# Kernel optimization log

Hardware: AMD Instinct MI355X
Metric: run time of the kernel (lower is better)

## Reference

```python
import jax, jax.numpy as jnp
import numpy as np

B, S, E, H = 4, 2048, 768, 12
D = E // H  # head_dim = 64


def setup_inputs() -> dict:
    key = jax.random.key(0)
    k1, k2, k3 = jax.random.split(key, 3)
    x = jax.random.normal(k1, (B, S, E), dtype=jnp.float32)
    # torch Linear(E, 3E): weight [3E, E]; we store transposed [E, 3E] for x @ W
    W_qkv = jax.random.normal(k2, (E, 3 * E), dtype=jnp.float32) * (E ** -0.5)
    b_qkv = jax.random.normal(k3, (3 * E,), dtype=jnp.float32) * 0.02
    return {"x": x, "W_qkv": W_qkv, "b_qkv": b_qkv}


def reference(x, W_qkv, b_qkv):
    n, length, embed_dim = x.shape
    qkv = x @ W_qkv + b_qkv                                   # [B, S, 3E]
    qkv = qkv.reshape(n, length, 3, H, D).transpose(2, 0, 3, 1, 4)  # [3, B, H, S, D]
    q, k, v = qkv[0], qkv[1], qkv[2]
    scores = jnp.einsum('bhsd,bhtd->bhst', q, k) * (D ** -0.5)  # [B, H, S, S]
    attn = jax.nn.softmax(scores, axis=-1)
    out = jnp.einsum('bhst,bhtd->bhsd', attn, v)               # [B, H, S, D]
    return out.transpose(0, 2, 1, 3).reshape(n, length, embed_dim)
```

## Files before the change

### kernel.cpp

```cpp
#include <hip/hip_runtime.h>
#include <cmath>

#define B_ 4
#define S_ 2048
#define E_ 768
#define H_ 12
#define D_ 64
#define NE3 (3*E_)
#define QKV_ELEMS ((size_t)B_*H_*S_*D_)

typedef __attribute__((ext_vector_type(8)))  short bf16x8;
typedef __attribute__((ext_vector_type(4)))  float f32x4;
typedef __attribute__((ext_vector_type(16))) float f32x16;

__device__ __forceinline__ unsigned short f2bf(float f) {
    union { float f; unsigned u; } v; v.f = f;
    return (unsigned short)((v.u + 0x7FFFu + ((v.u >> 16) & 1u)) >> 16);
}
__device__ __forceinline__ unsigned pk2(float a, float b) {
    return (unsigned)f2bf(a) | ((unsigned)f2bf(b) << 16);
}

__global__ __launch_bounds__(256)
void cvt_x(const float* __restrict__ x, unsigned short* __restrict__ xb)
{
    const size_t i = ((size_t)blockIdx.x * 256 + threadIdx.x) * 8;
    float4 a = *(const float4*)(x + i);
    float4 b = *(const float4*)(x + i + 4);
    ushort4 o0, o1;
    o0.x = f2bf(a.x); o0.y = f2bf(a.y); o0.z = f2bf(a.z); o0.w = f2bf(a.w);
    o1.x = f2bf(b.x); o1.y = f2bf(b.y); o1.z = f2bf(b.z); o1.w = f2bf(b.w);
    *(ushort4*)(xb + i)     = o0;
    *(ushort4*)(xb + i + 4) = o1;
}

__global__ __launch_bounds__(256)
void transpose_w(const float* __restrict__ W, unsigned short* __restrict__ Wt)
{
    __shared__ float t[32][33];
    const int tx = threadIdx.x & 31;
    const int ty = threadIdx.x >> 5;
    const int n0 = blockIdx.x * 32;
    const int k0 = blockIdx.y * 32;
    #pragma unroll
    for (int r = 0; r < 4; ++r)
        t[ty + 8*r][tx] = W[(size_t)(k0 + ty + 8*r) * NE3 + n0 + tx];
    __syncthreads();
    #pragma unroll
    for (int r = 0; r < 4; ++r)
        Wt[(size_t)(n0 + ty + 8*r) * E_ + k0 + tx] = f2bf(t[tx][ty + 8*r]);
}

__global__ __launch_bounds__(256, 2)
void qkv_gemm_mfma(const unsigned short* __restrict__ xb,
                   const unsigned short* __restrict__ Wt,
                   const float* __restrict__ bias,
                   unsigned short* __restrict__ qkv)
{
    __shared__ __align__(16) unsigned short As[128*64];
    __shared__ __align__(16) unsigned short Bs[128*64];

    const int tid  = threadIdx.x;
    const int lane = tid & 63;
    const int wave = tid >> 6;
    const int lo   = lane & 15;
    const int hi   = lane >> 4;
    const int wr   = wave >> 1;
    const int wc   = wave & 1;
    const int nstart = blockIdx.x * 128;
    const int mstart = blockIdx.y * 128;

    f32x4 acc[4][4];
    #pragma unroll
    for (int i = 0; i < 4; ++i)
        #pragma unroll
        for (int j = 0; j < 4; ++j) acc[i][j] = (f32x4){0.f,0.f,0.f,0.f};

    for (int k0 = 0; k0 < E_; k0 += 64) {
        __syncthreads();
        #pragma unroll
        for (int it = 0; it < 4; ++it) {
            const int cid = tid + it*256;
            const int row = cid >> 3, c = cid & 7;
            bf16x8 av = *(const bf16x8*)(xb + (size_t)(mstart + row)*E_ + k0 + c*8);
            *(bf16x8*)&As[row*64 + ((c ^ (row & 7)) * 8)] = av;
            bf16x8 bv = *(const bf16x8*)(Wt + (size_t)(nstart + row)*E_ + k0 + c*8);
            *(bf16x8*)&Bs[row*64 + ((c ^ (row & 7)) * 8)] = bv;
        }
        __syncthreads();

        #pragma unroll
        for (int ks = 0; ks < 2; ++ks) {
            const int c = ks*4 + hi;
            bf16x8 af[4], bfr[4];
            #pragma unroll
            for (int i = 0; i < 4; ++i) {
                const int ar = wr*64 + i*16 + lo;
                af[i] = *(const bf16x8*)&As[ar*64 + ((c ^ (ar & 7)) * 8)];
            }
            #pragma unroll
            for (int j = 0; j < 4; ++j) {
                const int br = wc*64 + j*16 + lo;
                bfr[j] = *(const bf16x8*)&Bs[br*64 + ((c ^ (br & 7)) * 8)];
            }
            #pragma unroll
            for (int i = 0; i < 4; ++i)
                #pragma unroll
                for (int j = 0; j < 4; ++j)
                    acc[i][j] = __builtin_amdgcn_mfma_f32_16x16x32_bf16(
                        af[i], bfr[j], acc[i][j], 0, 0, 0);
        }
    }

    #pragma unroll
    for (int j = 0; j < 4; ++j) {
        const int ncol = nstart + wc*64 + j*16 + lo;
        const int g  = ncol >> 6;
        const int cq = g / H_;
        const int h  = g % H_;
        const int d  = ncol & 63;
        const float bv = bias[ncol];
        const float qscale = (cq == 0) ? 0.125f : 1.0f;
        unsigned short* dst = qkv + (size_t)cq * QKV_ELEMS;
        #pragma unroll
        for (int i = 0; i < 4; ++i) {
            const int mbase = mstart + wr*64 + i*16 + hi*4;
            #pragma unroll
            for (int r = 0; r < 4; ++r) {
                const int m = mbase + r;
                const int b = m >> 11;
                const int s = m & 2047;
                dst[(((size_t)(b*H_ + h))*S_ + s)*D_ + d] =
                    f2bf((acc[i][j][r] + bv) * qscale);
            }
        }
    }
}

__global__ __launch_bounds__(256, 2)
void attn_mfma32(const unsigned short* __restrict__ qkv, float* __restrict__ out)
{
    __shared__ __align__(16) unsigned short Ks[64*64];
    __shared__ __align__(16) unsigned short Vt[64*64];

    const int tid  = threadIdx.x;
    const int lane = tid & 63;
    const int wave = tid >> 6;
    const int q32  = lane & 31;
    const int hi   = lane >> 5;
    const int qtile = blockIdx.x * 128;
    const int bh = blockIdx.y;
    const size_t base = (size_t)bh * S_ * D_;

    const unsigned short* Q = qkv;
    const unsigned short* K = qkv + QKV_ELEMS;
    const unsigned short* V = qkv + 2*QKV_ELEMS;

    bf16x8 qf[4];
    {
        const size_t qrow = base + (size_t)(qtile + wave*32 + q32) * D_;
        #pragma unroll
        for (int m = 0; m < 4; ++m)
            qf[m] = *(const bf16x8*)(Q + qrow + m*16 + hi*8);
    }

    f32x16 o0, o1;
    #pragma unroll
    for (int r = 0; r < 16; ++r) { o0[r] = 0.f; o1[r] = 0.f; }
    float m_run = -INFINITY, l_run = 0.f;

    for (int kc = 0; kc < S_; kc += 64) {
        __syncthreads();

        #pragma unroll
        for (int it = 0; it < 2; ++it) {
            const int cid = tid + it*256;
            const int key = cid >> 3, c = cid & 7;
            bf16x8 kv = *(const bf16x8*)(K + base + (size_t)(kc + key)*D_ + c*8);
            *(bf16x8*)&Ks[key*64 + ((c ^ (key & 7)) * 8)] = kv;
        }
        #pragma unroll
        for (int half = 0; half < 2; ++half) {
            const int d0 = wave*16 + half*8;
            bf16x8 vv = *(const bf16x8*)(V + base + (size_t)(kc + lane)*D_ + d0);
            #pragma unroll
            for (int j = 0; j < 8; ++j) {
                const int d = d0 + j;
                Vt[d*64 + (((lane >> 3) ^ (d & 7)) * 8) + (lane & 7)] =
                    (unsigned short)vv[j];
            }
        }
        __syncthreads();

        f32x16 sg[2];
        #pragma unroll
        for (int g = 0; g < 2; ++g) {
            f32x16 acc;
            #pragma unroll
            for (int r = 0; r < 16; ++r) acc[r] = 0.f;
            const int key = g*32 + q32;
            #pragma unroll
            for (int m = 0; m < 4; ++m) {
                const int c = m*2 + hi;
                bf16x8 kf = *(const bf16x8*)&Ks[key*64 + ((c ^ (key & 7)) * 8)];
                acc = __builtin_amdgcn_mfma_f32_32x32x16_bf16(kf, qf[m], acc, 0, 0, 0);
            }
            sg[g] = acc;
        }

        float mx = sg[0][0];
        #pragma unroll
        for (int r = 1; r < 16; ++r) mx = fmaxf(mx, sg[0][r]);
        #pragma unroll
        for (int r = 0; r < 16; ++r) mx = fmaxf(mx, sg[1][r]);
        mx = fmaxf(mx, __shfl_xor(mx, 32));
        const float mn = fmaxf(m_run, mx);
        const float alpha = __expf(m_run - mn);
        m_run = mn;

        float psum = 0.f;
        f32x16 p0v, p1v;
        #pragma unroll
        for (int r = 0; r < 16; ++r) { p0v[r] = __expf(sg[0][r] - mn); psum += p0v[r]; }
        #pragma unroll
        for (int r = 0; r < 16; ++r) { p1v[r] = __expf(sg[1][r] - mn); psum += p1v[r]; }
        psum += __shfl_xor(psum, 32);
        l_run = l_run * alpha + psum;

        #pragma unroll
        for (int r = 0; r < 16; ++r) { o0[r] *= alpha; o1[r] *= alpha; }

        unsigned U0[8], U1[8];
        #pragma unroll
        for (int c2 = 0; c2 < 8; ++c2) {
            asm("v_cvt_pk_bf16_f32 %0, %1, %2"
                : "=v"(U0[c2]) : "v"(p0v[2*c2]), "v"(p0v[2*c2+1]));
            asm("v_cvt_pk_bf16_f32 %0, %1, %2"
                : "=v"(U1[c2]) : "v"(p1v[2*c2]), "v"(p1v[2*c2+1]));
        }

        unsigned R0[2][2], R1[2][2];
        #pragma unroll
        for (int tb = 0; tb < 2; ++tb)
            #pragma unroll
            for (int w2 = 0; w2 < 2; ++w2) {
                unsigned s0 = hi ? U0[4*tb + w2] : U0[4*tb + 2 + w2];
                unsigned s1 = hi ? U1[4*tb + w2] : U1[4*tb + 2 + w2];
                R0[tb][w2] = (unsigned)__shfl_xor((int)s0, 32);
                R1[tb][w2] = (unsigned)__shfl_xor((int)s1, 32);
            }

        #pragma unroll
        for (int t = 0; t < 4; ++t) {
            const int tb = t & 1;
            union { unsigned w[4]; bf16x8 v; } pw;
            if (t < 2) {
                pw.w[0] = hi ? R0[tb][0] : U0[4*tb + 0];
                pw.w[1] = hi ? R0[tb][1] : U0[4*tb + 1];
                pw.w[2] = hi ? U0[4*tb + 2] : R0[tb][0];
                pw.w[3] = hi ? U0[4*tb + 3] : R0[tb][1];
            } else {
                pw.w[0] = hi ? R1[tb][0] : U1[4*tb + 0];
                pw.w[1] = hi ? R1[tb][1] : U1[4*tb + 1];
                pw.w[2] = hi ? U1[4*tb + 2] : R1[tb][0];
                pw.w[3] = hi ? U1[4*tb + 3] : R1[tb][1];
            }
            const int c = t*2 + hi;
            {
                const int d = q32;
                bf16x8 vf = *(const bf16x8*)&Vt[d*64 + ((c ^ (d & 7)) * 8)];
                o0 = __builtin_amdgcn_mfma_f32_32x32x16_bf16(vf, pw.v, o0, 0, 0, 0);
            }
            {
                const int d = 32 + q32;
                bf16x8 vf = *(const bf16x8*)&Vt[d*64 + ((c ^ (d & 7)) * 8)];
                o1 = __builtin_amdgcn_mfma_f32_32x32x16_bf16(vf, pw.v, o1, 0, 0, 0);
            }
        }
    }

    const int b = bh / H_;
    const int h = bh % H_;
    const float inv = 1.f / l_run;
    const int qglob = qtile + wave*32 + q32;
    float* obase = out + ((size_t)b*S_ + qglob)*E_ + h*64;
    #pragma unroll
    for (int rg = 0; rg < 4; ++rg) {
        float4 w0 = { o0[4*rg+0]*inv, o0[4*rg+1]*inv, o0[4*rg+2]*inv, o0[4*rg+3]*inv };
        *(float4*)(obase + rg*8 + hi*4) = w0;
        float4 w1 = { o1[4*rg+0]*inv, o1[4*rg+1]*inv, o1[4*rg+2]*inv, o1[4*rg+3]*inv };
        *(float4*)(obase + 32 + rg*8 + hi*4) = w1;
    }
}

extern "C" void kernel_launch(void* const* d_in, const int* in_sizes, int n_in,
                              void* d_out, int out_size, void* d_ws, size_t ws_size,
                              hipStream_t stream)
{
    (void)in_sizes; (void)n_in; (void)out_size; (void)ws_size;
    const float* x    = (const float*)d_in[0];
    const float* W    = (const float*)d_in[1];
    const float* bias = (const float*)d_in[2];
    float* out = (float*)d_out;

    unsigned short* qkv = (unsigned short*)d_ws;
    unsigned short* xb  = qkv + 3*QKV_ELEMS;
    unsigned short* Wtb = xb + (size_t)B_*S_*E_;

    cvt_x<<<(B_*S_*E_)/(256*8), 256, 0, stream>>>(x, xb);
    transpose_w<<<dim3(NE3/32, E_/32), 256, 0, stream>>>(W, Wtb);

    dim3 g1(NE3/128, (B_*S_)/128);
    qkv_gemm_mfma<<<g1, 256, 0, stream>>>(xb, Wtb, bias, qkv);

    dim3 g2(S_/128, B_*H_);
    attn_mfma32<<<g2, 256, 0, stream>>>(qkv, out);
}
```

Measured before the change: 140.3 us.

## Double-buffer K/V tiles in attention with register prefetch and faster softmax math

Result: no change. 138.3 us (-1.5%).

```diff
diff --git a/kernel.cpp b/kernel.cpp
--- a/kernel.cpp
+++ b/kernel.cpp
@@ -17,9 +17,14 @@
     union { float f; unsigned u; } v; v.f = f;
     return (unsigned short)((v.u + 0x7FFFu + ((v.u >> 16) & 1u)) >> 16);
 }
-__device__ __forceinline__ unsigned pk2(float a, float b) {
-    return (unsigned)f2bf(a) | ((unsigned)f2bf(b) << 16);
-}
+__device__ __forceinline__ float exp2_fast(float x) {
+    float r; asm("v_exp_f32 %0, %1" : "=v"(r) : "v"(x)); return r;
+}
+__device__ __forceinline__ float max3f(float a, float b, float c) {
+    float r; asm("v_max3_f32 %0, %1, %2, %3" : "=v"(r) : "v"(a), "v"(b), "v"(c));
+    return r;
+}
+#define LOG2E 1.44269504088896340736f
 
 __global__ __launch_bounds__(256)
 void cvt_x(const float* __restrict__ x, unsigned short* __restrict__ xb)
@@ -140,8 +145,8 @@
 __global__ __launch_bounds__(256, 2)
 void attn_mfma32(const unsigned short* __restrict__ qkv, float* __restrict__ out)
 {
-    __shared__ __align__(16) unsigned short Ks[64*64];
-    __shared__ __align__(16) unsigned short Vt[64*64];
+    __shared__ __align__(16) unsigned short Ks[2*64*64];
+    __shared__ __align__(16) unsigned short Vt[2*64*64];
 
     const int tid  = threadIdx.x;
     const int lane = tid & 63;
@@ -164,35 +169,52 @@
             qf[m] = *(const bf16x8*)(Q + qrow + m*16 + hi*8);
     }
 
+    const int kkey0 = tid >> 3,          kch0 = tid & 7;
+    const int kkey1 = (tid + 256) >> 3,  kch1 = (tid + 256) & 7;
+
+    bf16x8 kreg0, kreg1, vreg0, vreg1;
+    #define LOADKV(kc_) do {                                                         \
+        kreg0 = *(const bf16x8*)(K + base + (size_t)((kc_) + kkey0)*D_ + kch0*8);    \
+        kreg1 = *(const bf16x8*)(K + base + (size_t)((kc_) + kkey1)*D_ + kch1*8);    \
+        vreg0 = *(const bf16x8*)(V + base + (size_t)((kc_) + lane)*D_ + wave*16);    \
+        vreg1 = *(const bf16x8*)(V + base + (size_t)((kc_) + lane)*D_ + wave*16 + 8);\
+    } while (0)
+    #define STOREKV(buf_) do {                                                       \
+        const int o_ = (buf_) * 4096;                                                \
+        *(bf16x8*)&Ks[o_ + kkey0*64 + ((kch0 ^ (kkey0 & 7)) * 8)] = kreg0;           \
+        *(bf16x8*)&Ks[o_ + kkey1*64 + ((kch1 ^ (kkey1 & 7)) * 8)] = kreg1;           \
+        _Pragma("unroll")                                                            \
+        for (int j = 0; j < 8; ++j) {                                                \
+            const int d = wave*16 + j;                                               \
+            Vt[o_ + d*64 + (((lane >> 3) ^ (d & 7)) * 8) + (lane & 7)] =             \
+                (unsigned short)vreg0[j];                                            \
+        }                                                                            \
+        _Pragma("unroll")                                                            \
+        for (int j = 0; j < 8; ++j) {                                                \
+            const int d = wave*16 + 8 + j;                                           \
+            Vt[o_ + d*64 + (((lane >> 3) ^ (d & 7)) * 8) + (lane & 7)] =             \
+                (unsigned short)vreg1[j];                                            \
+        }                                                                            \
+    } while (0)
+
     f32x16 o0, o1;
     #pragma unroll
     for (int r = 0; r < 16; ++r) { o0[r] = 0.f; o1[r] = 0.f; }
     float m_run = -INFINITY, l_run = 0.f;
 
+    LOADKV(0);
+    STOREKV(0);
+    __syncthreads();
+    int cur = 0;
+
     for (int kc = 0; kc < S_; kc += 64) {
-        __syncthreads();
-
-        #pragma unroll
-        for (int it = 0; it < 2; ++it) {
-            const int cid = tid + it*256;
-            const int key = cid >> 3, c = cid & 7;
-            bf16x8 kv = *(const bf16x8*)(K + base + (size_t)(kc + key)*D_ + c*8);
-            *(bf16x8*)&Ks[key*64 + ((c ^ (key & 7)) * 8)] = kv;
-        }
-        #pragma unroll
-        for (int half = 0; half < 2; ++half) {
-            const int d0 = wave*16 + half*8;
-            bf16x8 vv = *(const bf16x8*)(V + base + (size_t)(kc + lane)*D_ + d0);
-            #pragma unroll
-            for (int j = 0; j < 8; ++j) {
-                const int d = d0 + j;
-                Vt[d*64 + (((lane >> 3) ^ (d & 7)) * 8) + (lane & 7)] =
-                    (unsigned short)vv[j];
-            }
-        }
-        __syncthreads();
+        const int nkc = (kc + 64 < S_) ? (kc + 64) : 0;
+        LOADKV(nkc);
+
+        const int o = cur * 4096;
 
         f32x16 sg[2];
+        __builtin_amdgcn_s_setprio(1);
         #pragma unroll
         for (int g = 0; g < 2; ++g) {
             f32x16 acc;
@@ -202,28 +224,42 @@
             #pragma unroll
             for (int m = 0; m < 4; ++m) {
                 const int c = m*2 + hi;
-                bf16x8 kf = *(const bf16x8*)&Ks[key*64 + ((c ^ (key & 7)) * 8)];
+                bf16x8 kf = *(const bf16x8*)&Ks[o + key*64 + ((c ^ (key & 7)) * 8)];
                 acc = __builtin_amdgcn_mfma_f32_32x32x16_bf16(kf, qf[m], acc, 0, 0, 0);
             }
             sg[g] = acc;
         }
-
-        float mx = sg[0][0];
-        #pragma unroll
-        for (int r = 1; r < 16; ++r) mx = fmaxf(mx, sg[0][r]);
-        #pragma unroll
-        for (int r = 0; r < 16; ++r) mx = fmaxf(mx, sg[1][r]);
+        __builtin_amdgcn_s_setprio(0);
+
+        float m0 = fmaxf(sg[0][0], sg[0][1]);
+        float m1 = fmaxf(sg[0][8], sg[0][9]);
+        float m2 = fmaxf(sg[1][0], sg[1][1]);
+        float m3 = fmaxf(sg[1][8], sg[1][9]);
+        #pragma unroll
+        for (int r = 2; r < 8; r += 2) {
+            m0 = max3f(m0, sg[0][r],   sg[0][r+1]);
+            m1 = max3f(m1, sg[0][r+8], sg[0][r+9]);
+            m2 = max3f(m2, sg[1][r],   sg[1][r+1]);
+            m3 = max3f(m3, sg[1][r+8], sg[1][r+9]);
+        }
+        float mx = fmaxf(fmaxf(m0, m1), fmaxf(m2, m3));
         mx = fmaxf(mx, __shfl_xor(mx, 32));
-        const float mn = fmaxf(m_run, mx);
-        const float alpha = __expf(m_run - mn);
+        const float mn    = fmaxf(m_run, mx);
+        const float alpha = exp2_fast((m_run - mn) * LOG2E);
         m_run = mn;
-
-        float psum = 0.f;
-        f32x16 p0v, p1v;
-        #pragma unroll
-        for (int r = 0; r < 16; ++r) { p0v[r] = __expf(sg[0][r] - mn); psum += p0v[r]; }
-        #pragma unroll
-        for (int r = 0; r < 16; ++r) { p1v[r] = __expf(sg[1][r] - mn); psum += p1v[r]; }
+        const float nmnL = -mn * LOG2E;
+
+        #pragma unroll
+        for (int r = 0; r < 16; ++r) sg[0][r] = exp2_fast(fmaf(sg[0][r], LOG2E, nmnL));
+        #pragma unroll
+        for (int r = 0; r < 16; ++r) sg[1][r] = exp2_fast(fmaf(sg[1][r], LOG2E, nmnL));
+
+        float a8[8];
+        #pragma unroll
+        for (int r = 0; r < 8; ++r) a8[r] = (sg[0][r] + sg[0][r+8]) + (sg[1][r] + sg[1][r+8]);
+        float a4_0 = a8[0] + a8[4], a4_1 = a8[1] + a8[5];
+        float a4_2 = a8[2] + a8[6], a4_3 = a8[3] + a8[7];
+        float psum = (a4_0 + a4_1) + (a4_2 + a4_3);
         psum += __shfl_xor(psum, 32);
         l_run = l_run * alpha + psum;
 
@@ -234,9 +270,9 @@
         #pragma unroll
         for (int c2 = 0; c2 < 8; ++c2) {
             asm("v_cvt_pk_bf16_f32 %0, %1, %2"
-                : "=v"(U0[c2]) : "v"(p0v[2*c2]), "v"(p0v[2*c2+1]));
+                : "=v"(U0[c2]) : "v"(sg[0][2*c2]), "v"(sg[0][2*c2+1]));
             asm("v_cvt_pk_bf16_f32 %0, %1, %2"
-                : "=v"(U1[c2]) : "v"(p1v[2*c2]), "v"(p1v[2*c2+1]));
+                : "=v"(U1[c2]) : "v"(sg[1][2*c2]), "v"(sg[1][2*c2+1]));
         }
 
         unsigned R0[2][2], R1[2][2];
@@ -250,6 +286,7 @@
                 R1[tb][w2] = (unsigned)__shfl_xor((int)s1, 32);
             }
 
+        __builtin_amdgcn_s_setprio(1);
         #pragma unroll
         for (int t = 0; t < 4; ++t) {
             const int tb = t & 1;
@@ -268,15 +305,20 @@
             const int c = t*2 + hi;
             {
                 const int d = q32;
-                bf16x8 vf = *(const bf16x8*)&Vt[d*64 + ((c ^ (d & 7)) * 8)];
+                bf16x8 vf = *(const bf16x8*)&Vt[o + d*64 + ((c ^ (d & 7)) * 8)];
                 o0 = __builtin_amdgcn_mfma_f32_32x32x16_bf16(vf, pw.v, o0, 0, 0, 0);
             }
             {
                 const int d = 32 + q32;
-                bf16x8 vf = *(const bf16x8*)&Vt[d*64 + ((c ^ (d & 7)) * 8)];
+                bf16x8 vf = *(const bf16x8*)&Vt[o + d*64 + ((c ^ (d & 7)) * 8)];
                 o1 = __builtin_amdgcn_mfma_f32_32x32x16_bf16(vf, pw.v, o1, 0, 0, 0);
             }
         }
+        __builtin_amdgcn_s_setprio(0);
+
+        STOREKV(cur ^ 1);
+        __syncthreads();
+        cur ^= 1;
     }
 
     const int b = bh / H_;
@@ -291,6 +333,8 @@
         float4 w1 = { o1[4*rg+0]*inv, o1[4*rg+1]*inv, o1[4*rg+2]*inv, o1[4*rg+3]*inv };
         *(float4*)(obase + 32 + rg*8 + hi*4) = w1;
     }
+    #undef LOADKV
+    #undef STOREKV
 }
 
 extern "C" void kernel_launch(void* const* d_in, const int* in_sizes, int n_in,
```
